# Kernel tuning notes

Hardware: AMD Instinct MI355X
Metric: run time of the kernel (lower is better)

The kernel has to match this reference:

```python
import jax, jax.numpy as jnp
import numpy as np

N = 50000       # nodes
E = 800000      # directed edges
F_IN = 128      # input feature dim
HID = 128       # hidden channels
DEPTH = 3


def glorot(key, shape):
    lim = (6.0 / (shape[0] + shape[-1])) ** 0.5
    return jax.random.uniform(key, shape, jnp.float32, -lim, lim)


def setup_inputs():
    key = jax.random.key(0)
    ks = jax.random.split(key, 20)
    inp = {
        "x": jax.random.normal(ks[0], (N, F_IN), jnp.float32),
        "edge_index": jax.random.randint(ks[1], (E, 2), 0, N),
        "y": jax.random.randint(ks[2], (N,), 0, 2),
    }
    dd = [(F_IN, HID), (HID, HID), (HID, HID), (HID, HID)]
    for i, (a, b) in enumerate(dd):
        inp[f"Wd{i}"] = glorot(ks[3 + i], (a, b))
        inp[f"bd{i}"] = jnp.zeros((b,), jnp.float32)
    for i in range(DEPTH):
        inp[f"Wp{i}"] = glorot(ks[7 + i], (2 * HID,))
        inp[f"bp{i}"] = jnp.zeros((), jnp.float32)
    du = [(2 * HID, HID), (2 * HID, HID), (2 * HID + F_IN, 1)]
    for i, (a, b) in enumerate(du):
        inp[f"Wu{i}"] = glorot(ks[10 + i], (a, b))
        inp[f"bu{i}"] = jnp.zeros((b,), jnp.float32)
    return inp


def gcn_conv(x, src, dst, ew, W, b):
    """GCNConv(improved=True): A_hat = A + 2I, symmetric normalization.
    ew masks invalid (deduped/padded) edges with 0."""
    n = x.shape[0]
    deg = 2.0 + jax.ops.segment_sum(ew, dst, num_segments=n)  # self-loop weight 2
    dinv = jax.lax.rsqrt(deg)
    xw = x @ W                                   # [n, out]
    norm = ew * dinv[src] * dinv[dst]            # [E]
    out = jax.ops.segment_sum(xw[src] * norm[:, None], dst, num_segments=n)
    out = out + (2.0 * dinv * dinv)[:, None] * xw  # self-loop contribution
    return out + b


def connected_components(src, dst, sel, n):
    """Weak CC over selected edges via min-label propagation + pointer jumping.
    Returns per-node label = min node index in its component."""
    s = jnp.where(sel, src, 0)  # masked edges become (0,0) self-loops
    d = jnp.where(sel, dst, 0)

    def body(state):
        lab, _ = state
        m = jnp.minimum(lab[s], lab[d])
        new = lab.at[s].min(m).at[d].min(m)
        new = new[new]
        new = new[new]
        return new, jnp.any(new != lab)

    lab, _ = jax.lax.while_loop(lambda st: st[1], body,
                                (jnp.arange(n), jnp.array(True)))
    return lab


def cluster_pool(x, src, dst, ew, Wp, bp):
    """ClusterPooling (eval mode): score edges, contract score>0.5 edges,
    merge components (sum of members scaled by mean intra-cluster edge score).
    Pooled graph keeps N slots; cluster ids are representative node indices."""
    n, hid = x.shape
    valid = (ew > 0) & (src != dst)
    s = jax.nn.sigmoid(x[src] @ Wp[:hid] + x[dst] @ Wp[hid:] + bp)  # [E]
    sel = valid & (s > 0.5)
    cluster = jax.lax.stop_gradient(connected_components(src, dst, sel, n))
    csrc = cluster[src]
    ssum = jax.ops.segment_sum(jnp.where(sel, s, 0.0), csrc, num_segments=n)
    scnt = jax.ops.segment_sum(sel.astype(x.dtype), csrc, num_segments=n)
    w = jnp.where(scnt > 0, ssum / jnp.maximum(scnt, 1.0), 1.0)  # singletons -> 1
    new_x = jax.ops.segment_sum(x, cluster, num_segments=n) * w[:, None]
    # remap edges to clusters, drop self-loops, coalesce duplicates (static shape)
    a = jnp.where(valid, cluster[src], n)
    b = jnp.where(valid, cluster[dst], n)
    loop = a == b
    a = jnp.where(loop, n, a)
    b = jnp.where(loop, n, b)
    order = jnp.lexsort((b, a))
    a, b = a[order], b[order]
    dup = jnp.concatenate([jnp.zeros((1,), bool),
                           (a[1:] == a[:-1]) & (b[1:] == b[:-1])])
    keep = (a < n) & (~dup)
    new_ew = keep.astype(x.dtype)
    a = jnp.where(keep, a, 0)
    b = jnp.where(keep, b, 0)
    return new_x, a, b, new_ew, (src, dst, ew, cluster)


def reference(x, edge_index, y,
              Wd0, bd0, Wd1, bd1, Wd2, bd2, Wd3, bd3,
              Wp0, bp0, Wp1, bp1, Wp2, bp2,
              Wu0, bu0, Wu1, bu1, Wu2, bu2):
    Wd = [Wd0, Wd1, Wd2, Wd3]; bd = [bd0, bd1, bd2, bd3]
    Wp = [Wp0, Wp1, Wp2]; bp = [bp0, bp1, bp2]
    Wu = [Wu0, Wu1, Wu2]; bu = [bu0, bu1, bu2]
    src = edge_index[:, 0]
    dst = edge_index[:, 1]
    ew = jnp.ones(src.shape[0], x.dtype)
    x_in = x
    memory, infos = [], []
    for i in range(DEPTH):
        x = jax.nn.relu(gcn_conv(x, src, dst, ew, Wd[i], bd[i]))
        memory.append(x)
        x, src, dst, ew, info = cluster_pool(x, src, dst, ew, Wp[i], bp[i])
        infos.append(info)
    memory[0] = jnp.concatenate([memory[0], x_in], axis=-1)
    x = gcn_conv(x, src, dst, ew, Wd[3], bd[3])
    for i in range(DEPTH):
        src, dst, ew, cluster = infos.pop()
        x = x[cluster]                                  # unpool
        x = jnp.concatenate([memory.pop(), x], axis=-1)  # skip connection
        x = gcn_conv(x, src, dst, ew, Wu[i], bu[i])
        if i < DEPTH - 1:
            x = jax.nn.relu(x)
    return jax.nn.sigmoid(x).ravel()
```

## Files before the change

kernel.cpp:

```cpp
#include <hip/hip_runtime.h>
#include <math.h>

#define NN 50000
#define EE 800000
#define HID 128
#define HSZ (1u<<21)
#define CC_ROUNDS 8
#define GN 196
#define WH 512
#define CH 128


static __device__ __forceinline__ float sigmoid_ref(float t) {
  if (t >= 0.f) { float e = expf(-t); return 1.f / (1.f + e); }
  float e = expf(t); return e / (1.f + e);
}

static __device__ __forceinline__ int edge_count(const int* cntp, int cnst) {
  return cntp ? *cntp : cnst;
}


__global__ void k_split_edges(const int* __restrict__ ei, int* __restrict__ s, int* __restrict__ d) {
  int T = gridDim.x*blockDim.x;
  for (int e = blockIdx.x*blockDim.x+threadIdx.x; e < EE; e += T) {
    s[e] = ei[2*e]; d[e] = ei[2*e+1];
  }
}

__global__ void k_degree(const int* __restrict__ eB, const int* cntp, int cnst, int* __restrict__ deg) {
  int n = edge_count(cntp, cnst);
  int T = gridDim.x*blockDim.x;
  for (int e = blockIdx.x*blockDim.x+threadIdx.x; e < n; e += T)
    atomicAdd(&deg[eB[e]], 1);
}

__global__ void k_scan1(const int* __restrict__ deg, int* __restrict__ rp, int* __restrict__ bsum) {
  __shared__ int sh[256];
  int tid = threadIdx.x; int i = blockIdx.x*256 + tid;
  int v = (i < NN) ? deg[i] : 0;
  sh[tid] = v; __syncthreads();
  for (int off = 1; off < 256; off <<= 1) {
    int t = (tid >= off) ? sh[tid-off] : 0;
    __syncthreads(); sh[tid] += t; __syncthreads();
  }
  if (i < NN) rp[i] = sh[tid] - v;
  if (tid == 255) bsum[blockIdx.x] = sh[255];
}

__global__ void k_scan2(int* __restrict__ bsum, int* __restrict__ rp, int nb) {
  __shared__ int sh[256];
  int tid = threadIdx.x;
  int v = (tid < nb) ? bsum[tid] : 0;
  sh[tid] = v; __syncthreads();
  for (int off = 1; off < 256; off <<= 1) {
    int t = (tid >= off) ? sh[tid-off] : 0;
    __syncthreads(); sh[tid] += t; __syncthreads();
  }
  if (tid < nb) bsum[tid] = sh[tid] - v;
  if (tid == 255) rp[NN] = sh[255];
}

__global__ void k_scan3(int* __restrict__ rp, const int* __restrict__ bsum, int* __restrict__ cursor,
                        const int* __restrict__ deg, float* __restrict__ dinv) {
  int i = blockIdx.x*256 + threadIdx.x;
  if (i < NN) {
    int r = rp[i] + bsum[blockIdx.x];
    rp[i] = r; cursor[i] = r;
    if (dinv) dinv[i] = (float)(1.0 / sqrt((double)(deg[i] + 2)));
  }
}

__global__ void k_csrfill(const int* __restrict__ eA, const int* __restrict__ eB,
                          const int* cntp, int cnst,
                          int* __restrict__ cursor, int* __restrict__ csr, int* __restrict__ dstE) {
  int n = edge_count(cntp, cnst);
  int T = gridDim.x*blockDim.x;
  for (int e = blockIdx.x*blockDim.x+threadIdx.x; e < n; e += T) {
    int d = eB[e];
    int p = atomicAdd(&cursor[d], 1);
    csr[p] = eA[e];
    dstE[p] = d;
  }
}


__global__ __launch_bounds__(256) void k_matmul(
    const float* __restrict__ A0, const int* __restrict__ idx0,
    const float* __restrict__ A1, const int* __restrict__ idx1,
    int K, const float* __restrict__ W, const float* __restrict__ dinv,
    float* __restrict__ C)
{
  __shared__ __align__(16) float As[64][68];
  __shared__ __align__(16) float Bs[64][HID];
  const int tid  = threadIdx.x;
  const int row0 = blockIdx.x * 64;
  const int colg = (tid & 31) * 4;
  const int rowg = (tid >> 5) * 8;
  float acc[8][4];
  #pragma unroll
  for (int i = 0; i < 8; ++i) { acc[i][0]=0.f; acc[i][1]=0.f; acc[i][2]=0.f; acc[i][3]=0.f; }

  for (int kc = 0; kc < K; kc += 64) {
    const float* Asrc = (kc < 128) ? A0 : A1;
    const int*   aidx = (kc < 128) ? idx0 : idx1;
    const int klocal  = (kc < 128) ? kc : (kc - 128);
    #pragma unroll
    for (int t = tid; t < 64*16; t += 256) {
      int r  = t >> 4;
      int k4 = (t & 15) << 2;
      int grow = row0 + r;
      if (grow >= NN) grow = NN - 1;
      int gr = aidx ? aidx[grow] : grow;
      float4 v = *(const float4*)(Asrc + (size_t)gr*HID + klocal + k4);
      As[k4+0][r] = v.x; As[k4+1][r] = v.y; As[k4+2][r] = v.z; As[k4+3][r] = v.w;
    }
    #pragma unroll
    for (int t = tid; t < 64*32; t += 256) {
      int kk = t >> 5;
      int c4 = (t & 31) << 2;
      *(float4*)&Bs[kk][c4] = *(const float4*)(W + (size_t)(kc+kk)*HID + c4);
    }
    __syncthreads();
    #pragma unroll 8
    for (int k = 0; k < 64; ++k) {
      float4 a0 = *(const float4*)&As[k][rowg];
      float4 a1 = *(const float4*)&As[k][rowg+4];
      float4 b  = *(const float4*)&Bs[k][colg];
      float ar[8] = {a0.x,a0.y,a0.z,a0.w,a1.x,a1.y,a1.z,a1.w};
      #pragma unroll
      for (int i = 0; i < 8; ++i) {
        acc[i][0] += ar[i]*b.x; acc[i][1] += ar[i]*b.y;
        acc[i][2] += ar[i]*b.z; acc[i][3] += ar[i]*b.w;
      }
    }
    __syncthreads();
  }
  #pragma unroll
  for (int i = 0; i < 8; ++i) {
    int r = row0 + rowg + i;
    if (r < NN) {
      float dv = dinv[r];
      *(float4*)(C + (size_t)r*HID + colg) =
        make_float4(acc[i][0]*dv, acc[i][1]*dv, acc[i][2]*dv, acc[i][3]*dv);
    }
  }
}

__global__ __launch_bounds__(256) void k_convinit(
    const float* __restrict__ xs, const float* __restrict__ dinv,
    const float* __restrict__ bias, float* __restrict__ out)
{
  int T = gridDim.x*blockDim.x;
  const float4* x4 = (const float4*)xs;
  float4* o4 = (float4*)out;
  const float4* b4 = (const float4*)bias;
  for (int i = blockIdx.x*blockDim.x+threadIdx.x; i < NN*HID/4; i += T) {
    int v = i >> 5;
    float c = 2.f*dinv[v];
    float4 xv = x4[i];
    float4 bb = b4[i & 31];
    o4[i] = make_float4(xv.x*c+bb.x, xv.y*c+bb.y, xv.z*c+bb.z, xv.w*c+bb.w);
  }
}

__global__ __launch_bounds__(256) void k_edgeagg(
    const float* __restrict__ xs, const int* __restrict__ csr, const int* __restrict__ dstE,
    const float* __restrict__ dinv, float* __restrict__ out,
    const int* cntp, int cnst)
{
  __shared__ int sh_s[8][CH];
  __shared__ int sh_d[8][CH];
  int n = edge_count(cntp, cnst);
  const int lane = threadIdx.x & 31;
  const int gsub = threadIdx.x >> 5;
  const int grp  = blockIdx.x*8 + gsub;
  const int p0   = grp * CH;
  if (p0 >= n) return;
  const int cnt = min(CH, n - p0);

  for (int j = lane; j < cnt; j += 32) {
    sh_s[gsub][j] = csr[p0 + j];
    sh_d[gsub][j] = dstE[p0 + j];
  }

  float4 pf[4];
  #pragma unroll
  for (int j = 0; j < 4; ++j) {
    if (j < cnt) {
      int s = sh_s[gsub][j];
      pf[j] = *(const float4*)(xs + (size_t)s*HID + lane*4);
    }
  }

  int cur = sh_d[gsub][0];
  float4 acc = make_float4(0.f,0.f,0.f,0.f);
  int flushes = 0;

  #pragma unroll 4
  for (int i = 0; i < cnt; ++i) {
    float4 xv = pf[i & 3];
    int jn = i + 4;
    if (jn < cnt) {
      int sn = sh_s[gsub][jn];
      pf[i & 3] = *(const float4*)(xs + (size_t)sn*HID + lane*4);
    }
    int d = sh_d[gsub][i];
    if (d != cur) {
      float dv = dinv[cur];
      float* o = out + (size_t)cur*HID + lane*4;
      if (flushes == 0) {
        atomicAdd(o+0, acc.x*dv); atomicAdd(o+1, acc.y*dv);
        atomicAdd(o+2, acc.z*dv); atomicAdd(o+3, acc.w*dv);
      } else {
        float4 ov = *(float4*)o;
        ov.x += acc.x*dv; ov.y += acc.y*dv; ov.z += acc.z*dv; ov.w += acc.w*dv;
        *(float4*)o = ov;
      }
      ++flushes;
      acc = make_float4(0.f,0.f,0.f,0.f);
      cur = d;
    }
    acc.x += xv.x; acc.y += xv.y; acc.z += xv.z; acc.w += xv.w;
  }
  float dv = dinv[cur];
  float* o = out + (size_t)cur*HID + lane*4;
  atomicAdd(o+0, acc.x*dv); atomicAdd(o+1, acc.y*dv);
  atomicAdd(o+2, acc.z*dv); atomicAdd(o+3, acc.w*dv);
}

__global__ void k_relu(float* __restrict__ x, int n4) {
  int T = gridDim.x*blockDim.x;
  float4* x4 = (float4*)x;
  for (int i = blockIdx.x*blockDim.x+threadIdx.x; i < n4; i += T) {
    float4 v = x4[i];
    v.x = fmaxf(v.x,0.f); v.y = fmaxf(v.y,0.f); v.z = fmaxf(v.z,0.f); v.w = fmaxf(v.w,0.f);
    x4[i] = v;
  }
}


__global__ __launch_bounds__(256) void k_node_ab(
    const float* __restrict__ h, const float* __restrict__ Wp,
    float* __restrict__ an, float* __restrict__ bn)
{
  int l = threadIdx.x & 63;
  int sub = threadIdx.x >> 6;
  float w0 = Wp[l], w1 = Wp[64+l], w2 = Wp[128+l], w3 = Wp[192+l];
  for (int g = blockIdx.x; g*4 < NN; g += gridDim.x) {
    int v = g*4 + sub;
    if (v >= NN) continue;
    float h0 = h[(size_t)v*HID + l];
    float h1 = h[(size_t)v*HID + 64 + l];
    float a = h0*w0 + h1*w1;
    float b = h0*w2 + h1*w3;
    #pragma unroll
    for (int off = 32; off; off >>= 1) { a += __shfl_down(a, off); b += __shfl_down(b, off); }
    if (l == 0) { an[v] = a; bn[v] = b; }
  }
}

__global__ void k_labinit(int* __restrict__ lab, int* __restrict__ flags,
                          int* __restrict__ selcnt, int* ecnt_next,
                          float* __restrict__ ssum2) {
  int i = blockIdx.x*256 + threadIdx.x;
  int T = gridDim.x*256;
  if (i < NN) lab[i] = i;
  for (int j = i; j < 2*NN; j += T) ssum2[j] = 0.f;
  if (i < 32) flags[i] = 0;
  if (i == 32) *selcnt = 0;
  if (i == 33 && ecnt_next) *ecnt_next = 0;
}

__global__ __launch_bounds__(256) void k_score_sel(
    const int* __restrict__ eA, const int* __restrict__ eB, const int* cntp, int cnst,
    const float* __restrict__ an, const float* __restrict__ bn, const float* __restrict__ bp,
    int* __restrict__ selA, int* __restrict__ selB, float* __restrict__ selS,
    int* __restrict__ selcnt)
{
  int n = edge_count(cntp, cnst);
  int T = gridDim.x*blockDim.x;
  int lane = threadIdx.x & 63;
  for (int e = blockIdx.x*blockDim.x+threadIdx.x; e < n; e += T) {
    int a = eA[e], b = eB[e];
    bool pred = false; float s = 0.f;
    if (a != b) {
      s = sigmoid_ref(an[a] + bn[b] + bp[0]);
      pred = s > 0.5f;
    }
    unsigned long long mask = __ballot(pred);
    if (mask) {
      int leader = __ffsll((long long)mask) - 1;
      int total  = __popcll(mask);
      int base = 0;
      if (lane == leader) base = atomicAdd(selcnt, total);
      base = __shfl(base, leader);
      if (pred) {
        int off = __popcll(mask & ((1ull << lane) - 1));
        selA[base+off] = a; selB[base+off] = b; selS[base+off] = s;
      }
    }
  }
}

__global__ __launch_bounds__(256) void k_hook(
    const int* __restrict__ selA, const int* __restrict__ selB, const int* __restrict__ selcnt,
    int* __restrict__ lab, const int* flagPrev, int* __restrict__ flagCur)
{
  if (flagPrev && *flagPrev == 0) return;
  int n = *selcnt;
  int T = gridDim.x*blockDim.x;
  bool changed = false;
  for (int i = blockIdx.x*blockDim.x+threadIdx.x; i < n; i += T) {
    int a = selA[i], b = selB[i];
    int la = lab[a], lb = lab[b];
    if (la == lb) continue;
    int pla = lab[la], plb = lab[lb];
    int m = min(pla, plb);
    if (la > m && lab[a] > m) atomicMin(&lab[a], m);
    if (lb > m && lab[b] > m) atomicMin(&lab[b], m);
    if (pla > m) atomicMin(&lab[la], m);
    if (plb > m) atomicMin(&lab[lb], m);
    changed = true;
  }
  unsigned long long m2 = __ballot(changed);
  if (m2 && (threadIdx.x & 63) == __ffsll((long long)m2) - 1) *flagCur = 1;
}

__global__ void k_jump(int* __restrict__ lab, const int* flagPrev, int* __restrict__ flagCur) {
  if (flagPrev && *flagPrev == 0) return;
  int i = blockIdx.x*256 + threadIdx.x;
  bool changed = false;
  if (i < NN) {
    int l0 = lab[i];
    int l = lab[l0]; l = lab[l]; l = lab[l];
    if (l < l0) { lab[i] = l; changed = true; }
  }
  unsigned long long m2 = __ballot(changed);
  if (m2 && (threadIdx.x & 63) == __ffsll((long long)m2) - 1) *flagCur = 1;
}

__global__ __launch_bounds__(256) void k_wsum(
    const int* __restrict__ selA, const float* __restrict__ selS,
    const int* __restrict__ selcnt, const int* __restrict__ cl,
    float* __restrict__ ssum, float* __restrict__ scnt)
{
  __shared__ int key[WH];
  __shared__ float vs[WH];
  __shared__ float vc[WH];
  int n = *selcnt;
  for (int i = threadIdx.x; i < WH; i += 256) { key[i] = -1; vs[i] = 0.f; vc[i] = 0.f; }
  __syncthreads();
  int T = gridDim.x*blockDim.x;
  for (int e = blockIdx.x*blockDim.x+threadIdx.x; e < n; e += T) {
    int c = cl[selA[e]];
    float s = selS[e];
    unsigned h = ((unsigned)c * 2654435761u) & (WH-1);
    bool done = false;
    for (int probe = 0; probe < 32; ++probe) {
      int k = key[h];
      if (k == c) { atomicAdd(&vs[h], s); atomicAdd(&vc[h], 1.f); done = true; break; }
      if (k == -1) {
        int old = atomicCAS(&key[h], -1, c);
        if (old == -1 || old == c) { atomicAdd(&vs[h], s); atomicAdd(&vc[h], 1.f); done = true; break; }
      }
      h = (h+1) & (WH-1);
    }
    if (!done) { atomicAdd(&ssum[c], s); atomicAdd(&scnt[c], 1.f); }
  }
  __syncthreads();
  for (int i = threadIdx.x; i < WH; i += 256) {
    if (key[i] >= 0) { atomicAdd(&ssum[key[i]], vs[i]); atomicAdd(&scnt[key[i]], vc[i]); }
  }
}

__global__ __launch_bounds__(128) void k_poolsum(const float* __restrict__ h,
                                                 const int* __restrict__ cl, float* __restrict__ p) {
  int f = threadIdx.x;
  int base = blockIdx.x * 64;
  int cur = -1; float acc = 0.f;
  for (int j = 0; j < 64; ++j) {
    int v = base + j;
    if (v >= NN) break;
    int c = cl[v];
    float x = h[(size_t)v*HID + f];
    if (c == cur) acc += x;
    else {
      if (cur >= 0) atomicAdd(&p[(size_t)cur*HID + f], acc);
      cur = c; acc = x;
    }
  }
  if (cur >= 0) atomicAdd(&p[(size_t)cur*HID + f], acc);
}

__global__ void k_poolscale(float* __restrict__ p, const float* __restrict__ ssum,
                            const float* __restrict__ scnt) {
  int T = gridDim.x*blockDim.x;
  float4* p4 = (float4*)p;
  for (int i = blockIdx.x*blockDim.x+threadIdx.x; i < NN*HID/4; i += T) {
    int r = i >> 5;
    float c = scnt[r];
    float w = (c > 0.f) ? ssum[r]/c : 1.f;
    float4 v = p4[i];
    v.x *= w; v.y *= w; v.z *= w; v.w *= w;
    p4[i] = v;
  }
}

__global__ __launch_bounds__(256) void k_contract(
    const int* __restrict__ eA, const int* __restrict__ eB, const int* cntp, int cnst,
    const int* __restrict__ cl, unsigned long long* __restrict__ tab,
    int* __restrict__ outA, int* __restrict__ outB, int* __restrict__ ocnt, int lev)
{
  int n = edge_count(cntp, cnst);
  int T = gridDim.x*blockDim.x;
  int lane = threadIdx.x & 63;
  for (int e = blockIdx.x*blockDim.x+threadIdx.x; e < n; e += T) {
    int s = eA[e], d = eB[e];
    bool keep = false; int a = 0, b = 0;
    if (s != d) {
      a = cl[s]; b = cl[d];
      if (a != b) {
        unsigned long long key = ((unsigned long long)lev << 34) |
                                 ((unsigned long long)a << 17) | (unsigned long long)b;
        unsigned long long hh = key * 0x9E3779B97F4A7C15ull;
        unsigned idx = (unsigned)(hh >> 40) & (HSZ - 1);
        while (true) {
          unsigned long long prev = atomicCAS(&tab[idx], ~0ull, key);
          if (prev == ~0ull) { keep = true; break; }
          if (prev == key) break;
          idx = (idx + 1) & (HSZ - 1);
        }
      }
    }
    unsigned long long mask = __ballot(keep);
    if (mask) {
      int leader = __ffsll((long long)mask) - 1;
      int total  = __popcll(mask);
      int base = 0;
      if (lane == leader) base = atomicAdd(ocnt, total);
      base = __shfl(base, leader);
      if (keep) {
        int off = __popcll(mask & ((1ull << lane) - 1));
        outA[base+off] = a; outB[base+off] = b;
      }
    }
  }
}


__global__ __launch_bounds__(256) void k_matvec384(
    const float* __restrict__ h1, const float* __restrict__ xin,
    const float* __restrict__ u1, const int* __restrict__ cl0,
    const float* __restrict__ Wu2, float* __restrict__ zw)
{
  int l = threadIdx.x & 63;
  int sub = threadIdx.x >> 6;
  float w0 = Wu2[l],     w1 = Wu2[64+l],  w2 = Wu2[128+l];
  float w3 = Wu2[192+l], w4 = Wu2[256+l], w5 = Wu2[320+l];
  for (int g = blockIdx.x; g*4 < NN; g += gridDim.x) {
    int v = g*4 + sub;
    if (v >= NN) continue;
    int gg = cl0[v];
    float s = h1[(size_t)v*HID + l]       * w0
            + h1[(size_t)v*HID + 64 + l]  * w1
            + xin[(size_t)v*HID + l]      * w2
            + xin[(size_t)v*HID + 64 + l] * w3
            + u1[(size_t)gg*HID + l]      * w4
            + u1[(size_t)gg*HID + 64 + l] * w5;
    #pragma unroll
    for (int off = 32; off; off >>= 1) s += __shfl_down(s, off);
    if (l == 0) zw[v] = s;
  }
}

__global__ void k_final(const float* __restrict__ zw, const int* __restrict__ rp,
                        const int* __restrict__ csr, const float* __restrict__ dinv,
                        const float* __restrict__ bu, float* __restrict__ out) {
  int T = gridDim.x*blockDim.x;
  for (int v = blockIdx.x*blockDim.x+threadIdx.x; v < NN; v += T) {
    float acc = 0.f;
    int p0 = rp[v], p1 = rp[v+1];
    for (int p = p0; p < p1; ++p) { int s = csr[p]; acc += zw[s]*dinv[s]; }
    float dv = dinv[v];
    float t = acc*dv + 2.f*dv*dv*zw[v] + bu[0];
    out[v] = sigmoid_ref(t);
  }
}


extern "C" void kernel_launch(void* const* d_in, const int* in_sizes, int n_in,
                              void* d_out, int out_size, void* d_ws, size_t ws_size,
                              hipStream_t stream) {
  const float* x_in = (const float*)d_in[0];
  const int*   ei   = (const int*)d_in[1];
  const float* Wd0 = (const float*)d_in[3];  const float* bd0 = (const float*)d_in[4];
  const float* Wd1 = (const float*)d_in[5];  const float* bd1 = (const float*)d_in[6];
  const float* Wd2 = (const float*)d_in[7];  const float* bd2 = (const float*)d_in[8];
  const float* Wd3 = (const float*)d_in[9];  const float* bd3 = (const float*)d_in[10];
  const float* Wp0 = (const float*)d_in[11]; const float* bp0 = (const float*)d_in[12];
  const float* Wp1 = (const float*)d_in[13]; const float* bp1 = (const float*)d_in[14];
  const float* Wp2 = (const float*)d_in[15]; const float* bp2 = (const float*)d_in[16];
  const float* Wu0 = (const float*)d_in[17]; const float* bu0 = (const float*)d_in[18];
  const float* Wu1 = (const float*)d_in[19]; const float* bu1 = (const float*)d_in[20];
  const float* Wu2 = (const float*)d_in[21]; const float* bu2 = (const float*)d_in[22];
  float* out = (float*)d_out;
  (void)in_sizes; (void)n_in; (void)out_size;

  char* wp = (char*)d_ws;
  auto alloc = [&](size_t bytes) -> void* {
    void* p = (void*)wp;
    wp += (bytes + 255) & ~(size_t)255;
    return p;
  };
  float* B[6]; for (int i = 0; i < 6; ++i) B[i] = (float*)alloc((size_t)NN*HID*4);
  int *eA[4], *eB[4];
  for (int i = 0; i < 4; ++i) { eA[i] = (int*)alloc((size_t)EE*4); eB[i] = (int*)alloc((size_t)EE*4); }
  int* cl[3];      for (int i = 0; i < 3; ++i) cl[i]    = (int*)alloc((size_t)NN*4);
  float* dinvL[4]; for (int i = 0; i < 4; ++i) dinvL[i] = (float*)alloc((size_t)NN*4);
  int* rpL[4]; int* csrL[4]; int* dstL[4];
  for (int i = 0; i < 4; ++i) {
    rpL[i]  = (int*)alloc((size_t)(NN+1)*4);
    csrL[i] = (int*)alloc((size_t)EE*4);
    dstL[i] = (int*)alloc((size_t)EE*4);
  }
  int*   selA = (int*)alloc((size_t)EE*4);
  int*   selB = (int*)alloc((size_t)EE*4);
  float* selS = (float*)alloc((size_t)EE*4);
  int* deg    = (int*)alloc((size_t)NN*4);
  int* cursor = (int*)alloc((size_t)NN*4);
  int* bsum   = (int*)alloc(256*4);
  float* an   = (float*)alloc((size_t)NN*4);
  float* bn   = (float*)alloc((size_t)NN*4);
  float* ssum = (float*)alloc((size_t)2*NN*4);
  float* scnt = ssum + NN;
  float* zw   = (float*)alloc((size_t)NN*4);
  int* selcnt = (int*)alloc(256);
  int* ecnt   = (int*)alloc(256);
  int* flags  = (int*)alloc(256);
  unsigned long long* tab = (unsigned long long*)alloc((size_t)HSZ*8);
  if ((size_t)(wp - (char*)d_ws) > ws_size) return;

  k_split_edges<<<1024,256,0,stream>>>(ei, eA[0], eB[0]);
  hipMemsetAsync(tab, 0xFF, (size_t)HSZ*8, stream);

  auto cntp = [&](int lev) -> const int* { return lev ? (ecnt + lev) : nullptr; };

  auto build_level = [&](int lev) {
    hipMemsetAsync(deg, 0, (size_t)NN*4, stream);
    k_degree<<<512,256,0,stream>>>(eB[lev], cntp(lev), EE, deg);
    k_scan1<<<GN,256,0,stream>>>(deg, rpL[lev], bsum);
    k_scan2<<<1,256,0,stream>>>(bsum, rpL[lev], GN);
    k_scan3<<<GN,256,0,stream>>>(rpL[lev], bsum, cursor, deg, dinvL[lev]);
    k_csrfill<<<512,256,0,stream>>>(eA[lev], eB[lev], cntp(lev), EE, cursor, csrL[lev], dstL[lev]);
  };

  const int GAGG = (EE + 8*CH - 1) / (8*CH);
  auto do_conv = [&](const float* A0, const int* i0, const float* A1, const int* i1, int K,
                     const float* W, const float* bias, int lev, float* xs, float* outp, int relu) {
    k_matmul<<<(NN+63)/64,256,0,stream>>>(A0, i0, A1, i1, K, W, dinvL[lev], xs);
    k_convinit<<<512,256,0,stream>>>(xs, dinvL[lev], bias, outp);
    k_edgeagg<<<GAGG,256,0,stream>>>(xs, csrL[lev], dstL[lev], dinvL[lev], outp, cntp(lev), EE);
    if (relu) k_relu<<<512,256,0,stream>>>(outp, NN*HID/4);
  };

  auto do_pool = [&](const float* h, int lev, int ci, float* p, const float* Wp, const float* bp) {
    k_node_ab<<<512,256,0,stream>>>(h, Wp, an, bn);
    k_labinit<<<GN,256,0,stream>>>(cl[ci], flags, selcnt, ecnt + lev + 1, ssum);
    k_score_sel<<<512,256,0,stream>>>(eA[lev], eB[lev], cntp(lev), EE, an, bn, bp,
                                      selA, selB, selS, selcnt);
    for (int r = 0; r < CC_ROUNDS; ++r) {
      const int* fp = r ? (flags + r - 1) : nullptr;
      k_hook<<<512,256,0,stream>>>(selA, selB, selcnt, cl[ci], fp, flags + r);
      k_jump<<<GN,256,0,stream>>>(cl[ci], fp, flags + r);
    }
    k_wsum<<<64,256,0,stream>>>(selA, selS, selcnt, cl[ci], ssum, scnt);
    hipMemsetAsync(p, 0, (size_t)NN*HID*4, stream);
    k_poolsum<<<(NN+63)/64,128,0,stream>>>(h, cl[ci], p);
    k_poolscale<<<1024,256,0,stream>>>(p, ssum, scnt);
    k_contract<<<512,256,0,stream>>>(eA[lev], eB[lev], cntp(lev), EE, cl[ci], tab,
                                     eA[lev+1], eB[lev+1], ecnt + lev + 1, lev);
  };

  build_level(0);
  do_conv(x_in, nullptr, nullptr, nullptr, 128, Wd0, bd0, 0, B[5], B[0], 1);
  do_pool(B[0], 0, 0, B[3], Wp0, bp0);
  build_level(1);
  do_conv(B[3], nullptr, nullptr, nullptr, 128, Wd1, bd1, 1, B[5], B[1], 1);
  do_pool(B[1], 1, 1, B[3], Wp1, bp1);
  build_level(2);
  do_conv(B[3], nullptr, nullptr, nullptr, 128, Wd2, bd2, 2, B[5], B[2], 1);
  do_pool(B[2], 2, 2, B[3], Wp2, bp2);
  build_level(3);
  do_conv(B[3], nullptr, nullptr, nullptr, 128, Wd3, bd3, 3, B[5], B[4], 0);
  do_conv(B[2], nullptr, B[4], cl[2], 256, Wu0, bu0, 2, B[5], B[3], 1);
  do_conv(B[1], nullptr, B[3], cl[1], 256, Wu1, bu1, 1, B[5], B[4], 1);
  k_matvec384<<<512,256,0,stream>>>(B[0], x_in, B[4], cl[0], Wu2, zw);
  k_final<<<512,256,0,stream>>>(zw, rpL[0], csrL[0], dinvL[0], bu2, out);
}
```

Measured before the change: 1.725 ms.

## Fuse conv init, relu and pool scaling into matmul; drop per-edge dst array

The self-loop plus bias initialisation is folded into the matmul epilogue. ReLU and the pool rescaling are applied lazily wherever the tensor is next read (matmul A-load, node_ab, poolsum, matvec384), which removes the k_convinit, k_relu and k_poolscale passes over the full N x 128 buffers. The per-edge destination array in CSR is replaced by a binary search on the row pointer plus a walk inside edgeagg, saving a write and a read of E ints per level. Edge-aggregation prefetch depth grows from 4 to 8 rows. The cost is extra per-element fmax and divide work in consumers, repeated relu and scale work when a cluster row is gathered several times, and a binary search per warp.

```diff
diff --git a/kernel.cpp b/kernel.cpp
--- a/kernel.cpp
+++ b/kernel.cpp
@@ -9,6 +9,7 @@
 #define GN 196
 #define WH 512
 #define CH 128
+#define PF 8
 
 
 static __device__ __forceinline__ float sigmoid_ref(float t) {
@@ -73,23 +74,22 @@
 
 __global__ void k_csrfill(const int* __restrict__ eA, const int* __restrict__ eB,
                           const int* cntp, int cnst,
-                          int* __restrict__ cursor, int* __restrict__ csr, int* __restrict__ dstE) {
+                          int* __restrict__ cursor, int* __restrict__ csr) {
   int n = edge_count(cntp, cnst);
   int T = gridDim.x*blockDim.x;
   for (int e = blockIdx.x*blockDim.x+threadIdx.x; e < n; e += T) {
-    int d = eB[e];
-    int p = atomicAdd(&cursor[d], 1);
+    int p = atomicAdd(&cursor[eB[e]], 1);
     csr[p] = eA[e];
-    dstE[p] = d;
   }
 }
 
 
 __global__ __launch_bounds__(256) void k_matmul(
-    const float* __restrict__ A0, const int* __restrict__ idx0,
-    const float* __restrict__ A1, const int* __restrict__ idx1,
+    const float* __restrict__ A0, const int* __restrict__ idx0, int reluA0,
+    const float* __restrict__ rsA, const float* __restrict__ rcA,
+    const float* __restrict__ A1, const int* __restrict__ idx1, int reluA1,
     int K, const float* __restrict__ W, const float* __restrict__ dinv,
-    float* __restrict__ C)
+    const float* __restrict__ bias, float* __restrict__ xs, float* __restrict__ outi)
 {
   __shared__ __align__(16) float As[64][68];
   __shared__ __align__(16) float Bs[64][HID];
@@ -102,9 +102,11 @@
   for (int i = 0; i < 8; ++i) { acc[i][0]=0.f; acc[i][1]=0.f; acc[i][2]=0.f; acc[i][3]=0.f; }
 
   for (int kc = 0; kc < K; kc += 64) {
-    const float* Asrc = (kc < 128) ? A0 : A1;
-    const int*   aidx = (kc < 128) ? idx0 : idx1;
-    const int klocal  = (kc < 128) ? kc : (kc - 128);
+    const bool first = (kc < 128);
+    const float* Asrc = first ? A0 : A1;
+    const int*   aidx = first ? idx0 : idx1;
+    const int    relu = first ? reluA0 : reluA1;
+    const int klocal  = first ? kc : (kc - 128);
     #pragma unroll
     for (int t = tid; t < 64*16; t += 256) {
       int r  = t >> 4;
@@ -113,6 +115,15 @@
       if (grow >= NN) grow = NN - 1;
       int gr = aidx ? aidx[grow] : grow;
       float4 v = *(const float4*)(Asrc + (size_t)gr*HID + klocal + k4);
+      if (relu) {
+        v.x = fmaxf(v.x,0.f); v.y = fmaxf(v.y,0.f);
+        v.z = fmaxf(v.z,0.f); v.w = fmaxf(v.w,0.f);
+      }
+      if (first && rsA) {
+        float c = rcA[gr];
+        float w = (c > 0.f) ? rsA[gr]/c : 1.f;
+        v.x *= w; v.y *= w; v.z *= w; v.w *= w;
+      }
       As[k4+0][r] = v.x; As[k4+1][r] = v.y; As[k4+2][r] = v.z; As[k4+3][r] = v.w;
     }
     #pragma unroll
@@ -136,41 +147,27 @@
     }
     __syncthreads();
   }
+  float4 bb = *(const float4*)(bias + colg);
   #pragma unroll
   for (int i = 0; i < 8; ++i) {
     int r = row0 + rowg + i;
     if (r < NN) {
       float dv = dinv[r];
-      *(float4*)(C + (size_t)r*HID + colg) =
-        make_float4(acc[i][0]*dv, acc[i][1]*dv, acc[i][2]*dv, acc[i][3]*dv);
-    }
-  }
-}
-
-__global__ __launch_bounds__(256) void k_convinit(
-    const float* __restrict__ xs, const float* __restrict__ dinv,
-    const float* __restrict__ bias, float* __restrict__ out)
-{
-  int T = gridDim.x*blockDim.x;
-  const float4* x4 = (const float4*)xs;
-  float4* o4 = (float4*)out;
-  const float4* b4 = (const float4*)bias;
-  for (int i = blockIdx.x*blockDim.x+threadIdx.x; i < NN*HID/4; i += T) {
-    int v = i >> 5;
-    float c = 2.f*dinv[v];
-    float4 xv = x4[i];
-    float4 bb = b4[i & 31];
-    o4[i] = make_float4(xv.x*c+bb.x, xv.y*c+bb.y, xv.z*c+bb.z, xv.w*c+bb.w);
+      float4 xv = make_float4(acc[i][0]*dv, acc[i][1]*dv, acc[i][2]*dv, acc[i][3]*dv);
+      *(float4*)(xs + (size_t)r*HID + colg) = xv;
+      float c2 = 2.f*dv;
+      *(float4*)(outi + (size_t)r*HID + colg) =
+        make_float4(xv.x*c2+bb.x, xv.y*c2+bb.y, xv.z*c2+bb.z, xv.w*c2+bb.w);
+    }
   }
 }
 
 __global__ __launch_bounds__(256) void k_edgeagg(
-    const float* __restrict__ xs, const int* __restrict__ csr, const int* __restrict__ dstE,
+    const float* __restrict__ xs, const int* __restrict__ csr, const int* __restrict__ rp,
     const float* __restrict__ dinv, float* __restrict__ out,
     const int* cntp, int cnst)
 {
   __shared__ int sh_s[8][CH];
-  __shared__ int sh_d[8][CH];
   int n = edge_count(cntp, cnst);
   const int lane = threadIdx.x & 31;
   const int gsub = threadIdx.x >> 5;
@@ -179,36 +176,36 @@
   if (p0 >= n) return;
   const int cnt = min(CH, n - p0);
 
-  for (int j = lane; j < cnt; j += 32) {
-    sh_s[gsub][j] = csr[p0 + j];
-    sh_d[gsub][j] = dstE[p0 + j];
-  }
-
-  float4 pf[4];
+  for (int j = lane; j < cnt; j += 32) sh_s[gsub][j] = csr[p0 + j];
+
+  int lo = 0, hi = NN;
+  while (lo + 1 < hi) { int mid = (lo + hi) >> 1; if (rp[mid] <= p0) lo = mid; else hi = mid; }
+  int v = lo;
+  int vend = rp[v+1];
+
+  float4 pf[PF];
   #pragma unroll
-  for (int j = 0; j < 4; ++j) {
+  for (int j = 0; j < PF; ++j) {
     if (j < cnt) {
       int s = sh_s[gsub][j];
       pf[j] = *(const float4*)(xs + (size_t)s*HID + lane*4);
     }
   }
 
-  int cur = sh_d[gsub][0];
   float4 acc = make_float4(0.f,0.f,0.f,0.f);
   int flushes = 0;
 
-  #pragma unroll 4
   for (int i = 0; i < cnt; ++i) {
-    float4 xv = pf[i & 3];
-    int jn = i + 4;
+    float4 xv = pf[i & (PF-1)];
+    int jn = i + PF;
     if (jn < cnt) {
       int sn = sh_s[gsub][jn];
-      pf[i & 3] = *(const float4*)(xs + (size_t)sn*HID + lane*4);
-    }
-    int d = sh_d[gsub][i];
-    if (d != cur) {
-      float dv = dinv[cur];
-      float* o = out + (size_t)cur*HID + lane*4;
+      pf[i & (PF-1)] = *(const float4*)(xs + (size_t)sn*HID + lane*4);
+    }
+    int p = p0 + i;
+    if (p >= vend) {
+      float dv = dinv[v];
+      float* o = out + (size_t)v*HID + lane*4;
       if (flushes == 0) {
         atomicAdd(o+0, acc.x*dv); atomicAdd(o+1, acc.y*dv);
         atomicAdd(o+2, acc.z*dv); atomicAdd(o+3, acc.w*dv);
@@ -219,24 +216,14 @@
       }
       ++flushes;
       acc = make_float4(0.f,0.f,0.f,0.f);
-      cur = d;
+      do { ++v; vend = rp[v+1]; } while (vend <= p);
     }
     acc.x += xv.x; acc.y += xv.y; acc.z += xv.z; acc.w += xv.w;
   }
-  float dv = dinv[cur];
-  float* o = out + (size_t)cur*HID + lane*4;
+  float dv = dinv[v];
+  float* o = out + (size_t)v*HID + lane*4;
   atomicAdd(o+0, acc.x*dv); atomicAdd(o+1, acc.y*dv);
   atomicAdd(o+2, acc.z*dv); atomicAdd(o+3, acc.w*dv);
-}
-
-__global__ void k_relu(float* __restrict__ x, int n4) {
-  int T = gridDim.x*blockDim.x;
-  float4* x4 = (float4*)x;
-  for (int i = blockIdx.x*blockDim.x+threadIdx.x; i < n4; i += T) {
-    float4 v = x4[i];
-    v.x = fmaxf(v.x,0.f); v.y = fmaxf(v.y,0.f); v.z = fmaxf(v.z,0.f); v.w = fmaxf(v.w,0.f);
-    x4[i] = v;
-  }
 }
 
 
@@ -250,8 +237,8 @@
   for (int g = blockIdx.x; g*4 < NN; g += gridDim.x) {
     int v = g*4 + sub;
     if (v >= NN) continue;
-    float h0 = h[(size_t)v*HID + l];
-    float h1 = h[(size_t)v*HID + 64 + l];
+    float h0 = fmaxf(h[(size_t)v*HID + l], 0.f);
+    float h1 = fmaxf(h[(size_t)v*HID + 64 + l], 0.f);
     float a = h0*w0 + h1*w1;
     float b = h0*w2 + h1*w3;
     #pragma unroll
@@ -383,7 +370,7 @@
     int v = base + j;
     if (v >= NN) break;
     int c = cl[v];
-    float x = h[(size_t)v*HID + f];
+    float x = fmaxf(h[(size_t)v*HID + f], 0.f);
     if (c == cur) acc += x;
     else {
       if (cur >= 0) atomicAdd(&p[(size_t)cur*HID + f], acc);
@@ -391,20 +378,6 @@
     }
   }
   if (cur >= 0) atomicAdd(&p[(size_t)cur*HID + f], acc);
-}
-
-__global__ void k_poolscale(float* __restrict__ p, const float* __restrict__ ssum,
-                            const float* __restrict__ scnt) {
-  int T = gridDim.x*blockDim.x;
-  float4* p4 = (float4*)p;
-  for (int i = blockIdx.x*blockDim.x+threadIdx.x; i < NN*HID/4; i += T) {
-    int r = i >> 5;
-    float c = scnt[r];
-    float w = (c > 0.f) ? ssum[r]/c : 1.f;
-    float4 v = p4[i];
-    v.x *= w; v.y *= w; v.z *= w; v.w *= w;
-    p4[i] = v;
-  }
 }
 
 __global__ __launch_bounds__(256) void k_contract(
@@ -462,12 +435,12 @@
     int v = g*4 + sub;
     if (v >= NN) continue;
     int gg = cl0[v];
-    float s = h1[(size_t)v*HID + l]       * w0
-            + h1[(size_t)v*HID + 64 + l]  * w1
-            + xin[(size_t)v*HID + l]      * w2
-            + xin[(size_t)v*HID + 64 + l] * w3
-            + u1[(size_t)gg*HID + l]      * w4
-            + u1[(size_t)gg*HID + 64 + l] * w5;
+    float s = fmaxf(h1[(size_t)v*HID + l], 0.f)       * w0
+            + fmaxf(h1[(size_t)v*HID + 64 + l], 0.f)  * w1
+            + xin[(size_t)v*HID + l]                  * w2
+            + xin[(size_t)v*HID + 64 + l]             * w3
+            + fmaxf(u1[(size_t)gg*HID + l], 0.f)      * w4
+            + fmaxf(u1[(size_t)gg*HID + 64 + l], 0.f) * w5;
     #pragma unroll
     for (int off = 32; off; off >>= 1) s += __shfl_down(s, off);
     if (l == 0) zw[v] = s;
@@ -518,11 +491,10 @@
   for (int i = 0; i < 4; ++i) { eA[i] = (int*)alloc((size_t)EE*4); eB[i] = (int*)alloc((size_t)EE*4); }
   int* cl[3];      for (int i = 0; i < 3; ++i) cl[i]    = (int*)alloc((size_t)NN*4);
   float* dinvL[4]; for (int i = 0; i < 4; ++i) dinvL[i] = (float*)alloc((size_t)NN*4);
-  int* rpL[4]; int* csrL[4]; int* dstL[4];
+  int* rpL[4]; int* csrL[4];
   for (int i = 0; i < 4; ++i) {
     rpL[i]  = (int*)alloc((size_t)(NN+1)*4);
     csrL[i] = (int*)alloc((size_t)EE*4);
-    dstL[i] = (int*)alloc((size_t)EE*4);
   }
   int*   selA = (int*)alloc((size_t)EE*4);
   int*   selB = (int*)alloc((size_t)EE*4);
@@ -552,16 +524,16 @@
     k_scan1<<<GN,256,0,stream>>>(deg, rpL[lev], bsum);
     k_scan2<<<1,256,0,stream>>>(bsum, rpL[lev], GN);
     k_scan3<<<GN,256,0,stream>>>(rpL[lev], bsum, cursor, deg, dinvL[lev]);
-    k_csrfill<<<512,256,0,stream>>>(eA[lev], eB[lev], cntp(lev), EE, cursor, csrL[lev], dstL[lev]);
+    k_csrfill<<<512,256,0,stream>>>(eA[lev], eB[lev], cntp(lev), EE, cursor, csrL[lev]);
   };
 
   const int GAGG = (EE + 8*CH - 1) / (8*CH);
-  auto do_conv = [&](const float* A0, const int* i0, const float* A1, const int* i1, int K,
-                     const float* W, const float* bias, int lev, float* xs, float* outp, int relu) {
-    k_matmul<<<(NN+63)/64,256,0,stream>>>(A0, i0, A1, i1, K, W, dinvL[lev], xs);
-    k_convinit<<<512,256,0,stream>>>(xs, dinvL[lev], bias, outp);
-    k_edgeagg<<<GAGG,256,0,stream>>>(xs, csrL[lev], dstL[lev], dinvL[lev], outp, cntp(lev), EE);
-    if (relu) k_relu<<<512,256,0,stream>>>(outp, NN*HID/4);
+  auto do_conv = [&](const float* A0, int reluA0, const float* rs, const float* rc,
+                     const float* A1, const int* i1, int reluA1, int K,
+                     const float* W, const float* bias, int lev, float* xs, float* outp) {
+    k_matmul<<<(NN+63)/64,256,0,stream>>>(A0, nullptr, reluA0, rs, rc,
+                                          A1, i1, reluA1, K, W, dinvL[lev], bias, xs, outp);
+    k_edgeagg<<<GAGG,256,0,stream>>>(xs, csrL[lev], rpL[lev], dinvL[lev], outp, cntp(lev), EE);
   };
 
   auto do_pool = [&](const float* h, int lev, int ci, float* p, const float* Wp, const float* bp) {
@@ -577,24 +549,23 @@
     k_wsum<<<64,256,0,stream>>>(selA, selS, selcnt, cl[ci], ssum, scnt);
     hipMemsetAsync(p, 0, (size_t)NN*HID*4, stream);
     k_poolsum<<<(NN+63)/64,128,0,stream>>>(h, cl[ci], p);
-    k_poolscale<<<1024,256,0,stream>>>(p, ssum, scnt);
     k_contract<<<512,256,0,stream>>>(eA[lev], eB[lev], cntp(lev), EE, cl[ci], tab,
                                      eA[lev+1], eB[lev+1], ecnt + lev + 1, lev);
   };
 
   build_level(0);
-  do_conv(x_in, nullptr, nullptr, nullptr, 128, Wd0, bd0, 0, B[5], B[0], 1);
+  do_conv(x_in, 0, nullptr, nullptr, nullptr, nullptr, 0, 128, Wd0, bd0, 0, B[5], B[0]);
   do_pool(B[0], 0, 0, B[3], Wp0, bp0);
   build_level(1);
-  do_conv(B[3], nullptr, nullptr, nullptr, 128, Wd1, bd1, 1, B[5], B[1], 1);
+  do_conv(B[3], 0, ssum, scnt, nullptr, nullptr, 0, 128, Wd1, bd1, 1, B[5], B[1]);
   do_pool(B[1], 1, 1, B[3], Wp1, bp1);
   build_level(2);
-  do_conv(B[3], nullptr, nullptr, nullptr, 128, Wd2, bd2, 2, B[5], B[2], 1);
+  do_conv(B[3], 0, ssum, scnt, nullptr, nullptr, 0, 128, Wd2, bd2, 2, B[5], B[2]);
   do_pool(B[2], 2, 2, B[3], Wp2, bp2);
   build_level(3);
-  do_conv(B[3], nullptr, nullptr, nullptr, 128, Wd3, bd3, 3, B[5], B[4], 0);
-  do_conv(B[2], nullptr, B[4], cl[2], 256, Wu0, bu0, 2, B[5], B[3], 1);
-  do_conv(B[1], nullptr, B[3], cl[1], 256, Wu1, bu1, 1, B[5], B[4], 1);
+  do_conv(B[3], 0, ssum, scnt, nullptr, nullptr, 0, 128, Wd3, bd3, 3, B[5], B[4]);
+  do_conv(B[2], 1, nullptr, nullptr, B[4], cl[2], 0, 256, Wu0, bu0, 2, B[5], B[3]);
+  do_conv(B[1], 1, nullptr, nullptr, B[3], cl[1], 1, 256, Wu1, bu1, 1, B[5], B[4]);
   k_matvec384<<<512,256,0,stream>>>(B[0], x_in, B[4], cl[0], Wu2, zw);
   k_final<<<512,256,0,stream>>>(zw, rpL[0], csrL[0], dinvL[0], bu2, out);
 }
```

Measured after the change: 2.453 ms. +42.2%, slower.
